# Kernel optimization log

Hardware: AMD Instinct MI355X
Metric: run time of the kernel (lower is better)

Reference implementation:

```python
import jax, jax.numpy as jnp
import numpy as np

B, S, D, H = 2, 2048, 1024, 16
DK = D // H

def setup_inputs() -> dict:
    key = jax.random.key(0)
    ks = jax.random.split(key, 5)
    scale = 1.0 / np.sqrt(D)
    return {
        "in_features": jax.random.normal(ks[0], (B, S, D), dtype=jnp.float32),
        "Wq": jax.random.normal(ks[1], (D, D), dtype=jnp.float32) * scale,
        "Wk": jax.random.normal(ks[2], (D, D), dtype=jnp.float32) * scale,
        "Wv": jax.random.normal(ks[3], (D, D), dtype=jnp.float32) * scale,
        "Wo": jax.random.normal(ks[4], (D, D), dtype=jnp.float32) * scale,
    }

def reference(in_features, Wq, Wk, Wv, Wo):
    b, s, d = in_features.shape
    # torch nn.Linear(bias=False): y = x @ W.T
    q = in_features @ Wq.T
    k = in_features @ Wk.T
    v = in_features @ Wv.T
    # [b, s, h*dk] -> [b, h, s, dk]
    def split_heads(x):
        return x.reshape(b, s, H, DK).transpose(0, 2, 1, 3)
    q, k, v = split_heads(q), split_heads(k), split_heads(v)
    scale = 1.0 / jnp.sqrt(jnp.asarray(DK, dtype=q.dtype))
    scores = jnp.einsum('bhqd,bhkd->bhqk', q, k) * scale
    causal = jnp.tril(jnp.ones((s, s), dtype=bool))
    scores = jnp.where(causal, scores, -jnp.inf)
    attn = jax.nn.softmax(scores, axis=-1)
    out = jnp.einsum('bhqk,bhkd->bhqd', attn, v)  # [b,h,s,dk]
    out = out.transpose(0, 2, 1, 3).reshape(b, s, d)
    return out @ Wo.T
```

## Files before the change

### kernel.cpp

```cpp
#include <hip/hip_runtime.h>
#include <hip/hip_bf16.h>


typedef __attribute__((ext_vector_type(4))) float f32x4;
typedef __attribute__((ext_vector_type(16))) float f32x16;
typedef __attribute__((ext_vector_type(8))) short bf16x8;

#define VSTR 2080

#if defined(__has_builtin)
#if __has_builtin(__builtin_amdgcn_permlane32_swap)
#define HAVE_PL32 1
#endif
#endif

__device__ __forceinline__ unsigned short f2bf(float f) {
  unsigned int u = __float_as_uint(f);
  u += 0x7fffu + ((u >> 16) & 1u);
  return (unsigned short)(u >> 16);
}

__device__ __forceinline__ unsigned int cvtpk_bf16(float lo, float hi) {
  unsigned int r;
  asm("v_cvt_pk_bf16_f32 %0, %1, %2" : "=v"(r) : "v"(lo), "v"(hi));
  return r;
}

__global__ void cast_f32_bf16(const float* __restrict__ src,
                              unsigned short* __restrict__ dst, int n4) {
  int i = blockIdx.x * blockDim.x + threadIdx.x;
  if (i >= n4) return;
  float4 v = ((const float4*)src)[i];
  ushort4 o = make_ushort4(f2bf(v.x), f2bf(v.y), f2bf(v.z), f2bf(v.w));
  ((ushort4*)dst)[i] = o;
}

__global__ void cast_w(const float* __restrict__ Wq, const float* __restrict__ Wk,
                       const float* __restrict__ Wv, const float* __restrict__ Wo,
                       unsigned short* __restrict__ Wqkvb, unsigned short* __restrict__ Wob,
                       int nw4) {
  int i = blockIdx.x * blockDim.x + threadIdx.x;
  int sel = i / nw4, r = i - sel * nw4;
  if (sel >= 4) return;
  const float* src = (sel == 0) ? Wq : (sel == 1) ? Wk : (sel == 2) ? Wv : Wo;
  unsigned short* dst = (sel < 3) ? (Wqkvb + (size_t)sel * 1024 * 1024) : Wob;
  float4 v = ((const float4*)src)[r];
  ushort4 o = make_ushort4(f2bf(v.x), f2bf(v.y), f2bf(v.z), f2bf(v.w));
  ((ushort4*)dst)[r] = o;
}

typedef __attribute__((address_space(1))) const void gas_t;
typedef __attribute__((address_space(3))) void las_t;

__device__ __forceinline__ void gld_lds16(const unsigned short* g, unsigned short* l) {
  __builtin_amdgcn_global_load_lds((gas_t*)g, (las_t*)l, 16, 0, 0);
}

__global__ __launch_bounds__(256)
void gemm_bt_f32(const unsigned short* __restrict__ A, const unsigned short* __restrict__ B,
                 float* __restrict__ C, int M, int N, int K) {
  __shared__ unsigned short As[128 * 32];
  __shared__ unsigned short Bs[128 * 32];
  const int tid = threadIdx.x;
  const int lane = tid & 63;
  const int wid = tid >> 6;
  const int wr = wid >> 1, wc = wid & 1;
  const int lr = lane & 15, lg = lane >> 4;
  const int m0 = blockIdx.x * 128, n0 = blockIdx.y * 128;

  f32x4 acc[4][4] = {};

  const int srow = tid >> 2;
  const int scol = (tid & 3) * 8;
  const unsigned short* Ag = A + (size_t)(m0 + srow) * K + scol;
  const unsigned short* Bg = B + (size_t)(n0 + srow) * K + scol;
  unsigned short* Al = &As[tid * 8];
  unsigned short* Bl = &Bs[tid * 8];

  for (int k0 = 0; k0 < K; k0 += 32) {
    gld_lds16(Ag + k0, Al);
    gld_lds16(Ag + k0 + (size_t)64 * K, Al + 2048);
    gld_lds16(Bg + k0, Bl);
    gld_lds16(Bg + k0 + (size_t)64 * K, Bl + 2048);
    asm volatile("s_waitcnt vmcnt(0)" ::: "memory");
    __syncthreads();

    bf16x8 af[4], bfr[4];
#pragma unroll
    for (int i = 0; i < 4; ++i)
      af[i] = *(const bf16x8*)&As[(wr * 64 + i * 16 + lr) * 32 + lg * 8];
#pragma unroll
    for (int j = 0; j < 4; ++j)
      bfr[j] = *(const bf16x8*)&Bs[(wc * 64 + j * 16 + lr) * 32 + lg * 8];
#pragma unroll
    for (int i = 0; i < 4; ++i)
#pragma unroll
      for (int j = 0; j < 4; ++j)
        acc[i][j] = __builtin_amdgcn_mfma_f32_16x16x32_bf16(af[i], bfr[j], acc[i][j], 0, 0, 0);
    __syncthreads();
  }

#pragma unroll
  for (int i = 0; i < 4; ++i) {
    const int row = m0 + wr * 64 + i * 16 + lg * 4;
#pragma unroll
    for (int j = 0; j < 4; ++j) {
      const int col = n0 + wc * 64 + j * 16 + lr;
#pragma unroll
      for (int r = 0; r < 4; ++r)
        C[(size_t)(row + r) * N + col] = acc[i][j][r];
    }
  }
}

__global__ __launch_bounds__(256)
void gemm_qkv(const unsigned short* __restrict__ A, const unsigned short* __restrict__ B,
              unsigned short* __restrict__ Qp, unsigned short* __restrict__ Kp,
              unsigned short* __restrict__ Vp) {
  const int K = 1024;
  __shared__ unsigned short As[128 * 32];
  __shared__ unsigned short Bs[128 * 32];
  const int tid = threadIdx.x;
  const int lane = tid & 63;
  const int wid = tid >> 6;
  const int wr = wid >> 1, wc = wid & 1;
  const int lr = lane & 15, lg = lane >> 4;
  const int m0 = blockIdx.x * 128, n0 = blockIdx.y * 128;

  f32x4 acc[4][4] = {};

  const int srow = tid >> 2;
  const int scol = (tid & 3) * 8;
  const unsigned short* Ag = A + (size_t)(m0 + srow) * K + scol;
  const unsigned short* Bg = B + (size_t)(n0 + srow) * K + scol;
  unsigned short* Al = &As[tid * 8];
  unsigned short* Bl = &Bs[tid * 8];

  for (int k0 = 0; k0 < K; k0 += 32) {
    gld_lds16(Ag + k0, Al);
    gld_lds16(Ag + k0 + (size_t)64 * K, Al + 2048);
    gld_lds16(Bg + k0, Bl);
    gld_lds16(Bg + k0 + (size_t)64 * K, Bl + 2048);
    asm volatile("s_waitcnt vmcnt(0)" ::: "memory");
    __syncthreads();

    bf16x8 af[4], bfr[4];
#pragma unroll
    for (int i = 0; i < 4; ++i)
      af[i] = *(const bf16x8*)&As[(wr * 64 + i * 16 + lr) * 32 + lg * 8];
#pragma unroll
    for (int j = 0; j < 4; ++j)
      bfr[j] = *(const bf16x8*)&Bs[(wc * 64 + j * 16 + lr) * 32 + lg * 8];
#pragma unroll
    for (int i = 0; i < 4; ++i)
#pragma unroll
      for (int j = 0; j < 4; ++j)
        acc[i][j] = __builtin_amdgcn_mfma_f32_16x16x32_bf16(af[i], bfr[j], acc[i][j], 0, 0, 0);
    __syncthreads();
  }

  const int region = blockIdx.y >> 3;
  const float qs = 0.125f * 1.44269504088896f;
#pragma unroll
  for (int i = 0; i < 4; ++i) {
    const int row0 = m0 + wr * 64 + i * 16 + lg * 4;
#pragma unroll
    for (int j = 0; j < 4; ++j) {
      const int col = n0 + wc * 64 + j * 16 + lr;
#pragma unroll
      for (int r = 0; r < 4; ++r) {
        const int row = row0 + r;
        float a = acc[i][j][r];
        const int b = row >> 11, s = row & 2047;
        if (region == 0) {
          Qp[(size_t)row * 1024 + col] = f2bf(a * qs);
        } else {
          const int c = col & 1023, h = c >> 6, d = c & 63;
          unsigned short* dst = (region == 1) ? Kp : Vp;
          dst[(size_t)((b * 16 + h) * 2048 + s) * 64 + d] = f2bf(a);
        }
      }
    }
  }
}

__global__ __launch_bounds__(256)
void transpose_vp(const unsigned short* __restrict__ Vp, unsigned short* __restrict__ VTp) {
  __shared__ __align__(16) unsigned short t[64 * 64];
  const int tid = threadIdx.x;
  const int bh = blockIdx.y;
  const int s0 = blockIdx.x * 64;
#pragma unroll
  for (int it = 0; it < 2; ++it) {
    int idx = it * 256 + tid;
    int r = idx >> 3, c8 = (idx & 7) * 8;
    bf16x8 v = *(const bf16x8*)(Vp + ((size_t)(bh * 2048 + s0 + r)) * 64 + c8);
    int sw = ((r & 7) ^ ((r >> 3) & 7)) * 8;
    *(bf16x8*)&t[r * 64 + (c8 ^ sw)] = v;
  }
  __syncthreads();
#pragma unroll
  for (int it = 0; it < 2; ++it) {
    int idx = it * 256 + tid;
    int d = idx >> 3, s8 = (idx & 7) * 8;
    unsigned short tmp[8];
#pragma unroll
    for (int j = 0; j < 8; ++j) {
      int row = s8 + j;
      int sw = ((row & 7) ^ ((row >> 3) & 7)) * 8;
      tmp[j] = t[row * 64 + ((d & ~7) ^ sw) + (d & 7)];
    }
    *(bf16x8*)(VTp + (size_t)(bh * 64 + d) * VSTR + s0 + s8) = *(bf16x8*)tmp;
  }
}

__global__ __launch_bounds__(256, 2)
void attn14(const unsigned short* __restrict__ Qp, const unsigned short* __restrict__ Kp,
            const unsigned short* __restrict__ VTp, unsigned short* __restrict__ O) {
  const int tid = threadIdx.x;
  const int w = tid >> 6;
  const int lane = tid & 63;
  const int l31 = lane & 31;
  const int hi = lane >> 5;
  const int blk = blockIdx.x;
  const int pair = blk >> 5;
  const int bh = blk & 31;
  const int b = bh >> 4, h = bh & 15;

  __shared__ float obuf[3][32][64];
  __shared__ float ml[4][32];

  const unsigned short* Qb = Qp + (size_t)b * 2048 * 1024 + h * 64;
  const unsigned short* Kb = Kp + (size_t)bh * 2048 * 64;
  const unsigned short* Vt = VTp + (size_t)bh * 64 * VSTR;

  for (int ph = 0; ph < 2; ++ph) {
    const int qp = ph ? (63 - pair) : pair;
    const int nt = (qp >> 1) + 1;
    const int t0 = (nt * w) >> 2;
    const int t1 = (nt * (w + 1)) >> 2;

    bf16x8 qf[4];
#pragma unroll
    for (int i = 0; i < 4; ++i)
      qf[i] = *(const bf16x8*)(Qb + (size_t)(qp * 32 + l31) * 1024 + 16 * i + 8 * hi);

    f32x16 o0, o1;
#pragma unroll
    for (int r = 0; r < 16; ++r) { o0[r] = 0.f; o1[r] = 0.f; }
    float Lp = 0.f;

    for (int t = t0; t < t1; ++t) {
      bf16x8 kfA[4], kfB[4];
#pragma unroll
      for (int i = 0; i < 4; ++i) {
        kfA[i] = *(const bf16x8*)(Kb + (size_t)(t * 64 + l31) * 64 + 16 * i + 8 * hi);
        kfB[i] = *(const bf16x8*)(Kb + (size_t)(t * 64 + 32 + l31) * 64 + 16 * i + 8 * hi);
      }
      bf16x8 vf[4][2];
#pragma unroll
      for (int s = 0; s < 4; ++s)
#pragma unroll
        for (int dh = 0; dh < 2; ++dh)
          vf[s][dh] = *(const bf16x8*)(Vt + (size_t)(dh * 32 + l31) * VSTR + t * 64 + s * 16 + 8 * hi);

      f32x16 stA, stB;
#pragma unroll
      for (int r = 0; r < 16; ++r) { stA[r] = 0.f; stB[r] = 0.f; }
      __builtin_amdgcn_s_setprio(1);
#pragma unroll
      for (int i = 0; i < 4; ++i) {
        stA = __builtin_amdgcn_mfma_f32_32x32x16_bf16(kfA[i], qf[i], stA, 0, 0, 0);
        stB = __builtin_amdgcn_mfma_f32_32x32x16_bf16(kfB[i], qf[i], stB, 0, 0, 0);
      }
      __builtin_amdgcn_s_setprio(0);

      if (t == nt - 1) {
        const int d0 = t * 64 - qp * 32;
#pragma unroll
        for (int r = 0; r < 16; ++r) {
          int kvi = (r & 3) + 8 * (r >> 2) + 4 * hi;
          if (kvi + d0 > l31)      stA[r] = -3.0e38f;
          if (kvi + d0 + 32 > l31) stB[r] = -3.0e38f;
        }
      }

      float pA[16], pB[16];
      float rs = 0.f;
#pragma unroll
      for (int r = 0; r < 16; ++r) {
        pA[r] = exp2f(stA[r]);
        pB[r] = exp2f(stB[r]);
        rs += pA[r] + pB[r];
      }
      Lp += rs;

      unsigned int pwA[8], pwB[8];
#pragma unroll
      for (int g = 0; g < 4; ++g) {
        pwA[2 * g]     = cvtpk_bf16(pA[4 * g],     pA[4 * g + 1]);
        pwA[2 * g + 1] = cvtpk_bf16(pA[4 * g + 2], pA[4 * g + 3]);
        pwB[2 * g]     = cvtpk_bf16(pB[4 * g],     pB[4 * g + 1]);
        pwB[2 * g + 1] = cvtpk_bf16(pB[4 * g + 2], pB[4 * g + 3]);
      }
#pragma unroll
      for (int s = 0; s < 4; ++s) {
        const unsigned int* pw = (s < 2) ? pwA : pwB;
        const int c = s & 1;
        unsigned int a0 = pw[4 * c], a1 = pw[4 * c + 1];
        unsigned int b0 = pw[4 * c + 2], b1 = pw[4 * c + 3];
        union { unsigned int u[4]; bf16x8 v; } af;
#ifdef HAVE_PL32
        auto r0 = __builtin_amdgcn_permlane32_swap(a0, b0, false, false);
        auto r1 = __builtin_amdgcn_permlane32_swap(a1, b1, false, false);
        af.u[0] = r0[0]; af.u[2] = r0[1];
        af.u[1] = r1[0]; af.u[3] = r1[1];
#else
        unsigned int sa0 = __shfl_xor(a0, 32), sa1 = __shfl_xor(a1, 32);
        unsigned int sb0 = __shfl_xor(b0, 32), sb1 = __shfl_xor(b1, 32);
        af.u[0] = hi ? sb0 : a0;
        af.u[1] = hi ? sb1 : a1;
        af.u[2] = hi ? b0  : sa0;
        af.u[3] = hi ? b1  : sa1;
#endif
        __builtin_amdgcn_s_setprio(1);
        o0 = __builtin_amdgcn_mfma_f32_32x32x16_bf16(af.v, vf[s][0], o0, 0, 0, 0);
        o1 = __builtin_amdgcn_mfma_f32_32x32x16_bf16(af.v, vf[s][1], o1, 0, 0, 0);
        __builtin_amdgcn_s_setprio(0);
      }
    }

    float Ltot = Lp + __shfl_xor(Lp, 32);
    if (!hi) ml[w][l31] = Ltot;
    if (w != 0) {
#pragma unroll
      for (int r = 0; r < 16; ++r) {
        int qr = (r & 3) + 8 * (r >> 2) + 4 * hi;
        obuf[w - 1][qr][l31]      = o0[r];
        obuf[w - 1][qr][32 + l31] = o1[r];
      }
    }
    __syncthreads();
    if (w == 0) {
#pragma unroll
      for (int r = 0; r < 16; ++r) {
        int qr = (r & 3) + 8 * (r >> 2) + 4 * hi;
        float L = ml[0][qr] + ml[1][qr] + ml[2][qr] + ml[3][qr];
        float inv = 1.0f / L;
        float v0 = o0[r] + obuf[0][qr][l31] + obuf[1][qr][l31] + obuf[2][qr][l31];
        float v1 = o1[r] + obuf[0][qr][32 + l31] + obuf[1][qr][32 + l31] + obuf[2][qr][32 + l31];
        size_t base = (size_t)(b * 2048 + qp * 32 + qr) * 1024 + h * 64;
        O[base + l31]      = f2bf(v0 * inv);
        O[base + 32 + l31] = f2bf(v1 * inv);
      }
    }
    __syncthreads();
  }
}

extern "C" void kernel_launch(void* const* d_in, const int* in_sizes, int n_in,
                              void* d_out, int out_size, void* d_ws, size_t ws_size,
                              hipStream_t stream) {
  const float* X  = (const float*)d_in[0];
  const float* Wq = (const float*)d_in[1];
  const float* Wk = (const float*)d_in[2];
  const float* Wv = (const float*)d_in[3];
  const float* Wo = (const float*)d_in[4];
  float* out = (float*)d_out;

  char* ws = (char*)d_ws;
  unsigned short* Xb    = (unsigned short*)(ws);
  unsigned short* Ob    = (unsigned short*)(ws);
  unsigned short* Wqkvb = (unsigned short*)(ws + (size_t)8  * 1024 * 1024);
  unsigned short* Wob   = (unsigned short*)(ws + (size_t)14 * 1024 * 1024);
  unsigned short* Qp    = (unsigned short*)(ws + (size_t)16 * 1024 * 1024);
  unsigned short* Kp    = (unsigned short*)(ws + (size_t)24 * 1024 * 1024);
  unsigned short* Vp    = (unsigned short*)(ws + (size_t)32 * 1024 * 1024);
  unsigned short* VTp   = (unsigned short*)(ws + (size_t)40 * 1024 * 1024);

  const int NX4 = (2 * 2048 * 1024) / 4;
  const int NW4 = (1024 * 1024) / 4;
  cast_f32_bf16<<<dim3((NX4 + 255) / 256), dim3(256), 0, stream>>>(X, Xb, NX4);
  cast_w<<<dim3((4 * NW4 + 255) / 256), dim3(256), 0, stream>>>(Wq, Wk, Wv, Wo, Wqkvb, Wob, NW4);

  gemm_qkv<<<dim3(32, 24), dim3(256), 0, stream>>>(Xb, Wqkvb, Qp, Kp, Vp);
  transpose_vp<<<dim3(32, 32), dim3(256), 0, stream>>>(Vp, VTp);
  attn14<<<dim3(1024), dim3(256), 0, stream>>>(Qp, Kp, VTp, Ob);
  gemm_bt_f32<<<dim3(32, 8), dim3(256), 0, stream>>>(Ob, Wob, out, 4096, 1024, 1024);
}
```

Before: 135.8 us.

## Process two 32-row query tiles per block so each K/V load is shared

The attention kernel now handles a 64-row query block, split into two 32-row tiles, per pass. It iterates over 32-key tiles so each K and V fragment load feeds MFMAs for both query tiles, and the grid shrinks from 1024 to 512 blocks. This cuts global K/V traffic per unit of work. In exchange it raises register pressure (four output accumulators) and LDS use (doubled obuf), and it halves the number of blocks, which may hurt occupancy and load balance.

```diff
diff --git a/kernel.cpp b/kernel.cpp
--- a/kernel.cpp
+++ b/kernel.cpp
@@ -215,7 +215,7 @@
 }
 
 __global__ __launch_bounds__(256, 2)
-void attn14(const unsigned short* __restrict__ Qp, const unsigned short* __restrict__ Kp,
+void attn15(const unsigned short* __restrict__ Qp, const unsigned short* __restrict__ Kp,
             const unsigned short* __restrict__ VTp, unsigned short* __restrict__ O) {
   const int tid = threadIdx.x;
   const int w = tid >> 6;
@@ -223,121 +223,148 @@
   const int l31 = lane & 31;
   const int hi = lane >> 5;
   const int blk = blockIdx.x;
-  const int pair = blk >> 5;
+  const int jp = blk >> 5;
   const int bh = blk & 31;
   const int b = bh >> 4, h = bh & 15;
 
-  __shared__ float obuf[3][32][64];
-  __shared__ float ml[4][32];
+  __shared__ float obuf[3][2][32][64];
+  __shared__ float ml[4][2][32];
 
   const unsigned short* Qb = Qp + (size_t)b * 2048 * 1024 + h * 64;
   const unsigned short* Kb = Kp + (size_t)bh * 2048 * 64;
   const unsigned short* Vt = VTp + (size_t)bh * 64 * VSTR;
 
   for (int ph = 0; ph < 2; ++ph) {
-    const int qp = ph ? (63 - pair) : pair;
-    const int nt = (qp >> 1) + 1;
+    const int j = ph ? (31 - jp) : jp;
+    const int qt0 = 2 * j, qt1 = 2 * j + 1;
+    const int nt = 2 * j + 2;
     const int t0 = (nt * w) >> 2;
     const int t1 = (nt * (w + 1)) >> 2;
 
-    bf16x8 qf[4];
-#pragma unroll
-    for (int i = 0; i < 4; ++i)
-      qf[i] = *(const bf16x8*)(Qb + (size_t)(qp * 32 + l31) * 1024 + 16 * i + 8 * hi);
-
-    f32x16 o0, o1;
-#pragma unroll
-    for (int r = 0; r < 16; ++r) { o0[r] = 0.f; o1[r] = 0.f; }
-    float Lp = 0.f;
+    bf16x8 qf0[4], qf1[4];
+#pragma unroll
+    for (int i = 0; i < 4; ++i) {
+      qf0[i] = *(const bf16x8*)(Qb + (size_t)(qt0 * 32 + l31) * 1024 + 16 * i + 8 * hi);
+      qf1[i] = *(const bf16x8*)(Qb + (size_t)(qt1 * 32 + l31) * 1024 + 16 * i + 8 * hi);
+    }
+
+    f32x16 o00, o01, o10, o11;
+#pragma unroll
+    for (int r = 0; r < 16; ++r) { o00[r] = 0.f; o01[r] = 0.f; o10[r] = 0.f; o11[r] = 0.f; }
+    float Lp0 = 0.f, Lp1 = 0.f;
 
     for (int t = t0; t < t1; ++t) {
-      bf16x8 kfA[4], kfB[4];
+      bf16x8 kf[4];
+#pragma unroll
+      for (int i = 0; i < 4; ++i)
+        kf[i] = *(const bf16x8*)(Kb + (size_t)(t * 32 + l31) * 64 + 16 * i + 8 * hi);
+      bf16x8 vf[2][2];
+#pragma unroll
+      for (int c = 0; c < 2; ++c)
+#pragma unroll
+        for (int dh = 0; dh < 2; ++dh)
+          vf[c][dh] = *(const bf16x8*)(Vt + (size_t)(dh * 32 + l31) * VSTR + t * 32 + c * 16 + 8 * hi);
+
+      f32x16 st0, st1;
+#pragma unroll
+      for (int r = 0; r < 16; ++r) { st0[r] = 0.f; st1[r] = 0.f; }
+      __builtin_amdgcn_s_setprio(1);
 #pragma unroll
       for (int i = 0; i < 4; ++i) {
-        kfA[i] = *(const bf16x8*)(Kb + (size_t)(t * 64 + l31) * 64 + 16 * i + 8 * hi);
-        kfB[i] = *(const bf16x8*)(Kb + (size_t)(t * 64 + 32 + l31) * 64 + 16 * i + 8 * hi);
-      }
-      bf16x8 vf[4][2];
-#pragma unroll
-      for (int s = 0; s < 4; ++s)
-#pragma unroll
-        for (int dh = 0; dh < 2; ++dh)
-          vf[s][dh] = *(const bf16x8*)(Vt + (size_t)(dh * 32 + l31) * VSTR + t * 64 + s * 16 + 8 * hi);
-
-      f32x16 stA, stB;
-#pragma unroll
-      for (int r = 0; r < 16; ++r) { stA[r] = 0.f; stB[r] = 0.f; }
-      __builtin_amdgcn_s_setprio(1);
-#pragma unroll
-      for (int i = 0; i < 4; ++i) {
-        stA = __builtin_amdgcn_mfma_f32_32x32x16_bf16(kfA[i], qf[i], stA, 0, 0, 0);
-        stB = __builtin_amdgcn_mfma_f32_32x32x16_bf16(kfB[i], qf[i], stB, 0, 0, 0);
+        st0 = __builtin_amdgcn_mfma_f32_32x32x16_bf16(kf[i], qf0[i], st0, 0, 0, 0);
+        st1 = __builtin_amdgcn_mfma_f32_32x32x16_bf16(kf[i], qf1[i], st1, 0, 0, 0);
       }
       __builtin_amdgcn_s_setprio(0);
 
-      if (t == nt - 1) {
-        const int d0 = t * 64 - qp * 32;
-#pragma unroll
-        for (int r = 0; r < 16; ++r) {
-          int kvi = (r & 3) + 8 * (r >> 2) + 4 * hi;
-          if (kvi + d0 > l31)      stA[r] = -3.0e38f;
-          if (kvi + d0 + 32 > l31) stB[r] = -3.0e38f;
+      {
+        const int dd0 = (t - qt0) * 32;
+        const int dd1 = (t - qt1) * 32;
+        if (dd0 >= 0) {
+#pragma unroll
+          for (int r = 0; r < 16; ++r) {
+            int kvi = (r & 3) + 8 * (r >> 2) + 4 * hi;
+            if (kvi + dd0 > l31) st0[r] = -3.0e38f;
+          }
         }
-      }
-
-      float pA[16], pB[16];
-      float rs = 0.f;
+        if (dd1 >= 0) {
+#pragma unroll
+          for (int r = 0; r < 16; ++r) {
+            int kvi = (r & 3) + 8 * (r >> 2) + 4 * hi;
+            if (kvi + dd1 > l31) st1[r] = -3.0e38f;
+          }
+        }
+      }
+
+      float p0[16], p1[16];
+      float rs0 = 0.f, rs1 = 0.f;
 #pragma unroll
       for (int r = 0; r < 16; ++r) {
-        pA[r] = exp2f(stA[r]);
-        pB[r] = exp2f(stB[r]);
-        rs += pA[r] + pB[r];
-      }
-      Lp += rs;
-
-      unsigned int pwA[8], pwB[8];
+        p0[r] = exp2f(st0[r]);
+        p1[r] = exp2f(st1[r]);
+        rs0 += p0[r];
+        rs1 += p1[r];
+      }
+      Lp0 += rs0;
+      Lp1 += rs1;
+
+      unsigned int pw0[8], pw1[8];
 #pragma unroll
       for (int g = 0; g < 4; ++g) {
-        pwA[2 * g]     = cvtpk_bf16(pA[4 * g],     pA[4 * g + 1]);
-        pwA[2 * g + 1] = cvtpk_bf16(pA[4 * g + 2], pA[4 * g + 3]);
-        pwB[2 * g]     = cvtpk_bf16(pB[4 * g],     pB[4 * g + 1]);
-        pwB[2 * g + 1] = cvtpk_bf16(pB[4 * g + 2], pB[4 * g + 3]);
-      }
-#pragma unroll
-      for (int s = 0; s < 4; ++s) {
-        const unsigned int* pw = (s < 2) ? pwA : pwB;
-        const int c = s & 1;
-        unsigned int a0 = pw[4 * c], a1 = pw[4 * c + 1];
-        unsigned int b0 = pw[4 * c + 2], b1 = pw[4 * c + 3];
-        union { unsigned int u[4]; bf16x8 v; } af;
+        pw0[2 * g]     = cvtpk_bf16(p0[4 * g],     p0[4 * g + 1]);
+        pw0[2 * g + 1] = cvtpk_bf16(p0[4 * g + 2], p0[4 * g + 3]);
+        pw1[2 * g]     = cvtpk_bf16(p1[4 * g],     p1[4 * g + 1]);
+        pw1[2 * g + 1] = cvtpk_bf16(p1[4 * g + 2], p1[4 * g + 3]);
+      }
+#pragma unroll
+      for (int c = 0; c < 2; ++c) {
+        unsigned int a00 = pw0[4 * c], a01 = pw0[4 * c + 1];
+        unsigned int b00 = pw0[4 * c + 2], b01 = pw0[4 * c + 3];
+        unsigned int a10 = pw1[4 * c], a11 = pw1[4 * c + 1];
+        unsigned int b10 = pw1[4 * c + 2], b11 = pw1[4 * c + 3];
+        union { unsigned int u[4]; bf16x8 v; } af0, af1;
 #ifdef HAVE_PL32
-        auto r0 = __builtin_amdgcn_permlane32_swap(a0, b0, false, false);
-        auto r1 = __builtin_amdgcn_permlane32_swap(a1, b1, false, false);
-        af.u[0] = r0[0]; af.u[2] = r0[1];
-        af.u[1] = r1[0]; af.u[3] = r1[1];
+        auto r00 = __builtin_amdgcn_permlane32_swap(a00, b00, false, false);
+        auto r01 = __builtin_amdgcn_permlane32_swap(a01, b01, false, false);
+        auto r10 = __builtin_amdgcn_permlane32_swap(a10, b10, false, false);
+        auto r11 = __builtin_amdgcn_permlane32_swap(a11, b11, false, false);
+        af0.u[0] = r00[0]; af0.u[2] = r00[1];
+        af0.u[1] = r01[0]; af0.u[3] = r01[1];
+        af1.u[0] = r10[0]; af1.u[2] = r10[1];
+        af1.u[1] = r11[0]; af1.u[3] = r11[1];
 #else
-        unsigned int sa0 = __shfl_xor(a0, 32), sa1 = __shfl_xor(a1, 32);
-        unsigned int sb0 = __shfl_xor(b0, 32), sb1 = __shfl_xor(b1, 32);
-        af.u[0] = hi ? sb0 : a0;
-        af.u[1] = hi ? sb1 : a1;
-        af.u[2] = hi ? b0  : sa0;
-        af.u[3] = hi ? b1  : sa1;
+        unsigned int s00 = __shfl_xor(a00, 32), s01 = __shfl_xor(a01, 32);
+        unsigned int t00 = __shfl_xor(b00, 32), t01 = __shfl_xor(b01, 32);
+        unsigned int s10 = __shfl_xor(a10, 32), s11 = __shfl_xor(a11, 32);
+        unsigned int t10 = __shfl_xor(b10, 32), t11 = __shfl_xor(b11, 32);
+        af0.u[0] = hi ? t00 : a00;
+        af0.u[1] = hi ? t01 : a01;
+        af0.u[2] = hi ? b00 : s00;
+        af0.u[3] = hi ? b01 : s01;
+        af1.u[0] = hi ? t10 : a10;
+        af1.u[1] = hi ? t11 : a11;
+        af1.u[2] = hi ? b10 : s10;
+        af1.u[3] = hi ? b11 : s11;
 #endif
         __builtin_amdgcn_s_setprio(1);
-        o0 = __builtin_amdgcn_mfma_f32_32x32x16_bf16(af.v, vf[s][0], o0, 0, 0, 0);
-        o1 = __builtin_amdgcn_mfma_f32_32x32x16_bf16(af.v, vf[s][1], o1, 0, 0, 0);
+        o00 = __builtin_amdgcn_mfma_f32_32x32x16_bf16(af0.v, vf[c][0], o00, 0, 0, 0);
+        o01 = __builtin_amdgcn_mfma_f32_32x32x16_bf16(af0.v, vf[c][1], o01, 0, 0, 0);
+        o10 = __builtin_amdgcn_mfma_f32_32x32x16_bf16(af1.v, vf[c][0], o10, 0, 0, 0);
+        o11 = __builtin_amdgcn_mfma_f32_32x32x16_bf16(af1.v, vf[c][1], o11, 0, 0, 0);
         __builtin_amdgcn_s_setprio(0);
       }
     }
 
-    float Ltot = Lp + __shfl_xor(Lp, 32);
-    if (!hi) ml[w][l31] = Ltot;
+    float Lt0 = Lp0 + __shfl_xor(Lp0, 32);
+    float Lt1 = Lp1 + __shfl_xor(Lp1, 32);
+    if (!hi) { ml[w][0][l31] = Lt0; ml[w][1][l31] = Lt1; }
     if (w != 0) {
 #pragma unroll
       for (int r = 0; r < 16; ++r) {
         int qr = (r & 3) + 8 * (r >> 2) + 4 * hi;
-        obuf[w - 1][qr][l31]      = o0[r];
-        obuf[w - 1][qr][32 + l31] = o1[r];
+        obuf[w - 1][0][qr][l31]      = o00[r];
+        obuf[w - 1][0][qr][32 + l31] = o01[r];
+        obuf[w - 1][1][qr][l31]      = o10[r];
+        obuf[w - 1][1][qr][32 + l31] = o11[r];
       }
     }
     __syncthreads();
@@ -345,13 +372,19 @@
 #pragma unroll
       for (int r = 0; r < 16; ++r) {
         int qr = (r & 3) + 8 * (r >> 2) + 4 * hi;
-        float L = ml[0][qr] + ml[1][qr] + ml[2][qr] + ml[3][qr];
-        float inv = 1.0f / L;
-        float v0 = o0[r] + obuf[0][qr][l31] + obuf[1][qr][l31] + obuf[2][qr][l31];
-        float v1 = o1[r] + obuf[0][qr][32 + l31] + obuf[1][qr][32 + l31] + obuf[2][qr][32 + l31];
-        size_t base = (size_t)(b * 2048 + qp * 32 + qr) * 1024 + h * 64;
-        O[base + l31]      = f2bf(v0 * inv);
-        O[base + 32 + l31] = f2bf(v1 * inv);
+        float L0 = ml[0][0][qr] + ml[1][0][qr] + ml[2][0][qr] + ml[3][0][qr];
+        float L1 = ml[0][1][qr] + ml[1][1][qr] + ml[2][1][qr] + ml[3][1][qr];
+        float i0 = 1.0f / L0, i1 = 1.0f / L1;
+        float v00 = o00[r] + obuf[0][0][qr][l31]      + obuf[1][0][qr][l31]      + obuf[2][0][qr][l31];
+        float v01 = o01[r] + obuf[0][0][qr][32 + l31] + obuf[1][0][qr][32 + l31] + obuf[2][0][qr][32 + l31];
+        float v10 = o10[r] + obuf[0][1][qr][l31]      + obuf[1][1][qr][l31]      + obuf[2][1][qr][l31];
+        float v11 = o11[r] + obuf[0][1][qr][32 + l31] + obuf[1][1][qr][32 + l31] + obuf[2][1][qr][32 + l31];
+        size_t base0 = (size_t)(b * 2048 + qt0 * 32 + qr) * 1024 + h * 64;
+        size_t base1 = (size_t)(b * 2048 + qt1 * 32 + qr) * 1024 + h * 64;
+        O[base0 + l31]      = f2bf(v00 * i0);
+        O[base0 + 32 + l31] = f2bf(v01 * i0);
+        O[base1 + l31]      = f2bf(v10 * i1);
+        O[base1 + 32 + l31] = f2bf(v11 * i1);
       }
     }
     __syncthreads();
@@ -385,6 +418,6 @@
 
   gemm_qkv<<<dim3(32, 24), dim3(256), 0, stream>>>(Xb, Wqkvb, Qp, Kp, Vp);
   transpose_vp<<<dim3(32, 32), dim3(256), 0, stream>>>(Vp, VTp);
-  attn14<<<dim3(1024), dim3(256), 0, stream>>>(Qp, Kp, VTp, Ob);
+  attn15<<<dim3(512), dim3(256), 0, stream>>>(Qp, Kp, VTp, Ob);
   gemm_bt_f32<<<dim3(32, 8), dim3(256), 0, stream>>>(Ob, Wob, out, 4096, 1024, 1024);
 }
```

Result: faster. 119.0 us (-12.4%).
